# Kernel optimization log

Hardware: AMD Instinct MI355X
Metric: run time of the kernel (lower is better)

## Reference

```python
import jax, jax.numpy as jnp
import numpy as np

H = 128
NUM_IN = 384
B, N, K = 4, 2048, 48
SCALE = 30.0
EPS = 1e-5


def _layernorm(x, gamma, beta):
    mu = jnp.mean(x, axis=-1, keepdims=True)
    var = jnp.mean(jnp.square(x - mu), axis=-1, keepdims=True)
    return (x - mu) * jax.lax.rsqrt(var + EPS) * gamma + beta


def setup_inputs() -> dict:
    key = jax.random.key(0)
    ks = jax.random.split(key, 12)
    s = lambda fan_in: 1.0 / np.sqrt(fan_in)
    inp = {
        "h_V": jax.random.normal(ks[0], (B, N, H), jnp.float32),
        "h_E": jax.random.normal(ks[1], (B, N, K, NUM_IN), jnp.float32),
        "mask_V": jnp.ones((B, N), jnp.float32),
        "mask_attend": jnp.ones((B, N, K), jnp.float32),
        # message MLP
        "W1": jax.random.uniform(ks[2], (H + NUM_IN, H), jnp.float32, -s(H + NUM_IN), s(H + NUM_IN)),
        "b1": jnp.zeros((H,), jnp.float32),
        "W2": jax.random.uniform(ks[3], (H, H), jnp.float32, -s(H), s(H)),
        "b2": jnp.zeros((H,), jnp.float32),
        "W3": jax.random.uniform(ks[4], (H, H), jnp.float32, -s(H), s(H)),
        "b3": jnp.zeros((H,), jnp.float32),
        # layernorms
        "g1": jnp.ones((H,), jnp.float32), "be1": jnp.zeros((H,), jnp.float32),
        "g2": jnp.ones((H,), jnp.float32), "be2": jnp.zeros((H,), jnp.float32),
        # FFN
        "Wi": jax.random.uniform(ks[5], (H, 4 * H), jnp.float32, -s(H), s(H)),
        "bi": jnp.zeros((4 * H,), jnp.float32),
        "Wo": jax.random.uniform(ks[6], (4 * H, H), jnp.float32, -s(4 * H), s(4 * H)),
        "bo": jnp.zeros((H,), jnp.float32),
        # rezero alpha (init 0.01)
        "alpha": jnp.array([0.01], jnp.float32),
    }
    return inp


def reference(h_V, h_E, mask_V, mask_attend, W1, b1, W2, b2, W3, b3,
              g1, be1, g2, be2, Wi, bi, Wo, bo, alpha):
    gelu = lambda x: jax.nn.gelu(x, approximate=False)
    # broadcast-concat node features onto each neighbor edge: [B,N,K,H+num_in]
    h_V_expand = jnp.broadcast_to(h_V[:, :, None, :], (*h_E.shape[:-1], h_V.shape[-1]))
    h_EV = jnp.concatenate([h_V_expand, h_E], axis=-1)
    # 3-layer message MLP
    h_message = gelu(jnp.einsum("bnkf,fh->bnkh", h_EV, W1) + b1)
    h_message = gelu(jnp.einsum("bnkh,hg->bnkg", h_message, W2) + b2)
    h_message = jnp.einsum("bnkg,gh->bnkh", h_message, W3) + b3
    h_message = mask_attend[..., None] * h_message
    # masked sum-reduce over neighbors
    dh = jnp.sum(h_message, axis=-2) / SCALE
    # residual (rezero) + LayerNorm  (dropout = identity in eval)
    h = _layernorm(alpha * dh + h_V, g1, be1)
    # position-wise FFN
    dh = gelu(h @ Wi + bi) @ Wo + bo
    h = _layernorm(alpha * dh + h, g2, be2)
    # node mask
    h = mask_V[..., None] * h
    return h
```

## Files before the change

### kernel.cpp

```cpp
#include <hip/hip_runtime.h>

#define LN_EPS 1e-5f
#define RSCALE (1.0f / 30.0f)

typedef short short8  __attribute__((ext_vector_type(8)));
typedef short short4v __attribute__((ext_vector_type(4)));
typedef float f32x4   __attribute__((ext_vector_type(4)));

__device__ __forceinline__ unsigned short f2bf(float f) {
    unsigned u = __builtin_bit_cast(unsigned, f);
    u = u + 0x7FFFu + ((u >> 16) & 1u);
    return (unsigned short)(u >> 16);
}

__device__ __forceinline__ float gelu_f(float x) {
    float u  = 0.7978845608028654f * (x + 0.044715f * x * x * x);
    float e  = __expf(-2.0f * fabsf(u));
    float t  = 1.0f - 2.0f * e / (1.0f + e);
    return 0.5f * x * (1.0f + copysignf(t, u));
}

__device__ __forceinline__ short8 cvt8(float4 a, float4 b) {
    short8 r;
    r[0] = (short)f2bf(a.x); r[1] = (short)f2bf(a.y);
    r[2] = (short)f2bf(a.z); r[3] = (short)f2bf(a.w);
    r[4] = (short)f2bf(b.x); r[5] = (short)f2bf(b.y);
    r[6] = (short)f2bf(b.z); r[7] = (short)f2bf(b.w);
    return r;
}

__device__ __forceinline__ f32x4 zero4() {
    f32x4 v; v.x = 0.f; v.y = 0.f; v.z = 0.f; v.w = 0.f; return v;
}

__global__ __launch_bounds__(256) void prep_w(
    const float* __restrict__ W1, const float* __restrict__ W2,
    const float* __restrict__ W3,
    unsigned short* __restrict__ w1t, unsigned short* __restrict__ w2t,
    unsigned short* __restrict__ w3t)
{
    int t = blockIdx.x * 256 + threadIdx.x;
    if (t < 65536) {
        int m = t & 127, k = t >> 7;
        w1t[m * 512 + k] = f2bf(W1[k * 128 + m]);
    } else if (t < 81920) {
        int u = t - 65536, m = u & 127, k = u >> 7;
        w2t[m * 128 + k] = f2bf(W2[k * 128 + m]);
    } else if (t < 98304) {
        int u = t - 81920, m = u & 127, k = u >> 7;
        w3t[m * 128 + k] = f2bf(W3[k * 128 + m]);
    }
}

__global__ __launch_bounds__(256, 2) void edge_mlp(
    const float* __restrict__ hV, const float* __restrict__ hE,
    const float* __restrict__ mAtt,
    const unsigned short* __restrict__ w1t, const unsigned short* __restrict__ w2t,
    const unsigned short* __restrict__ w3t,
    const float* __restrict__ b1, const float* __restrict__ b2,
    const float* __restrict__ b3, float* __restrict__ dh)
{
    __shared__ short Hs[4][48 * 128];

    const int tid  = threadIdx.x;
    const int wv   = tid >> 6;
    const int lane = tid & 63;
    const int ln   = lane & 15;
    const int kg   = lane >> 4;
    const int node = blockIdx.x * 4 + wv;
    short* Hw = &Hs[wv][0];

    f32x4 acc[8][3];

#pragma unroll
    for (int j = 0; j < 8; ++j) acc[j][0] = zero4();
#pragma unroll
    for (int ks = 0; ks < 4; ++ks) {
        const float* hp = hV + node * 128 + ks * 32 + kg * 8;
        float4 v0 = *(const float4*)hp;
        float4 v1 = *(const float4*)(hp + 4);
        short8 bf = cvt8(v0, v1);
#pragma unroll
        for (int j = 0; j < 8; ++j) {
            short8 af = *(const short8*)(w1t + (j * 16 + ln) * 512 + ks * 32 + kg * 8);
            acc[j][0] = __builtin_amdgcn_mfma_f32_16x16x32_bf16(af, bf, acc[j][0], 0, 0, 0);
        }
    }
#pragma unroll
    for (int j = 0; j < 8; ++j) { acc[j][1] = acc[j][0]; acc[j][2] = acc[j][0]; }

    float4 e0[3], e1[3];
#pragma unroll
    for (int i = 0; i < 3; ++i) {
        const float* p = hE + (node * 48 + 16 * i + ln) * 384 + kg * 8;
        e0[i] = *(const float4*)p;
        e1[i] = *(const float4*)(p + 4);
    }
    for (int ks = 4; ks < 16; ++ks) {
        float4 f0[3], f1[3];
        if (ks < 15) {
#pragma unroll
            for (int i = 0; i < 3; ++i) {
                const float* p = hE + (node * 48 + 16 * i + ln) * 384 + (ks - 3) * 32 + kg * 8;
                f0[i] = *(const float4*)p;
                f1[i] = *(const float4*)(p + 4);
            }
        }
        short8 bf[3];
#pragma unroll
        for (int i = 0; i < 3; ++i) bf[i] = cvt8(e0[i], e1[i]);
#pragma unroll
        for (int j = 0; j < 8; ++j) {
            short8 af = *(const short8*)(w1t + (j * 16 + ln) * 512 + ks * 32 + kg * 8);
#pragma unroll
            for (int i = 0; i < 3; ++i)
                acc[j][i] = __builtin_amdgcn_mfma_f32_16x16x32_bf16(af, bf[i], acc[j][i], 0, 0, 0);
        }
#pragma unroll
        for (int i = 0; i < 3; ++i) { e0[i] = f0[i]; e1[i] = f1[i]; }
    }

#pragma unroll
    for (int j = 0; j < 8; ++j) {
        const float4 bb = *(const float4*)(b1 + j * 16 + 4 * kg);
        const int blk0 = 2 * j + (kg >> 1);
        const int off  = 4 * (kg & 1);
#pragma unroll
        for (int i = 0; i < 3; ++i) {
            const int n = 16 * i + ln;
            short4v p;
            p.x = (short)f2bf(gelu_f(acc[j][i].x + bb.x));
            p.y = (short)f2bf(gelu_f(acc[j][i].y + bb.y));
            p.z = (short)f2bf(gelu_f(acc[j][i].z + bb.z));
            p.w = (short)f2bf(gelu_f(acc[j][i].w + bb.w));
            *(short4v*)&Hw[n * 128 + ((blk0 ^ (n & 7)) * 8) + off] = p;
        }
    }

    for (int L = 0; L < 2; ++L) {
        const unsigned short* wt = (L == 0) ? w2t : w3t;
        f32x4 a2[8][3];
#pragma unroll
        for (int j = 0; j < 8; ++j)
#pragma unroll
            for (int i = 0; i < 3; ++i) a2[j][i] = zero4();

#pragma unroll
        for (int c = 0; c < 4; ++c) {
            short8 hb[3];
#pragma unroll
            for (int i = 0; i < 3; ++i) {
                const int n = 16 * i + ln;
                const int blk = (c * 4 + kg) ^ (n & 7);
                hb[i] = *(const short8*)&Hw[n * 128 + blk * 8];
            }
#pragma unroll
            for (int j = 0; j < 8; ++j) {
                short8 af = *(const short8*)(wt + (j * 16 + ln) * 128 + c * 32 + kg * 8);
#pragma unroll
                for (int i = 0; i < 3; ++i)
                    a2[j][i] = __builtin_amdgcn_mfma_f32_16x16x32_bf16(af, hb[i], a2[j][i], 0, 0, 0);
            }
        }

        if (L == 0) {
#pragma unroll
            for (int j = 0; j < 8; ++j) {
                const float4 bb = *(const float4*)(b2 + j * 16 + 4 * kg);
                const int blk0 = 2 * j + (kg >> 1);
                const int off  = 4 * (kg & 1);
#pragma unroll
                for (int i = 0; i < 3; ++i) {
                    const int n = 16 * i + ln;
                    short4v p;
                    p.x = (short)f2bf(gelu_f(a2[j][i].x + bb.x));
                    p.y = (short)f2bf(gelu_f(a2[j][i].y + bb.y));
                    p.z = (short)f2bf(gelu_f(a2[j][i].z + bb.z));
                    p.w = (short)f2bf(gelu_f(a2[j][i].w + bb.w));
                    *(short4v*)&Hw[n * 128 + ((blk0 ^ (n & 7)) * 8) + off] = p;
                }
            }
        } else {
            float mk[3];
#pragma unroll
            for (int i = 0; i < 3; ++i) mk[i] = mAtt[node * 48 + 16 * i + ln];
#pragma unroll
            for (int j = 0; j < 8; ++j) {
                const float4 bb = *(const float4*)(b3 + j * 16 + 4 * kg);
                float s0 = 0.f, s1 = 0.f, s2 = 0.f, s3 = 0.f;
#pragma unroll
                for (int i = 0; i < 3; ++i) {
                    s0 += (a2[j][i].x + bb.x) * mk[i];
                    s1 += (a2[j][i].y + bb.y) * mk[i];
                    s2 += (a2[j][i].z + bb.z) * mk[i];
                    s3 += (a2[j][i].w + bb.w) * mk[i];
                }
#pragma unroll
                for (int off = 1; off < 16; off <<= 1) {
                    s0 += __shfl_xor(s0, off, 64);
                    s1 += __shfl_xor(s1, off, 64);
                    s2 += __shfl_xor(s2, off, 64);
                    s3 += __shfl_xor(s3, off, 64);
                }
                if (ln == 0) {
                    float4 o;
                    o.x = s0 * RSCALE; o.y = s1 * RSCALE;
                    o.z = s2 * RSCALE; o.w = s3 * RSCALE;
                    *(float4*)&dh[node * 128 + j * 16 + 4 * kg] = o;
                }
            }
        }
    }
}

__global__ __launch_bounds__(256, 2) void node_ffn(
    const float* __restrict__ hV, const float* __restrict__ dh,
    const float* __restrict__ maskV,
    const float* __restrict__ g1, const float* __restrict__ be1,
    const float* __restrict__ g2, const float* __restrict__ be2,
    const float* __restrict__ Wi, const float* __restrict__ bi,
    const float* __restrict__ Wo, const float* __restrict__ bo,
    const float* __restrict__ alphap, float* __restrict__ out)
{
    __shared__ float hbuf[16 * 132];
    __shared__ float hidb[16 * 516];
    __shared__ float obuf[16 * 132];

    const int tid = threadIdx.x;
    const float al = alphap[0];
    const int nb = blockIdx.x * 16;

    {
        const int m = tid >> 4, s = tid & 15;
        const int i0 = s * 8;
        const int base = (nb + m) * 128 + i0;
        float x[8];
        {
            float4 a0 = *(const float4*)(dh + base);
            float4 a1 = *(const float4*)(dh + base + 4);
            float4 v0 = *(const float4*)(hV + base);
            float4 v1 = *(const float4*)(hV + base + 4);
            x[0] = v0.x + al * a0.x; x[1] = v0.y + al * a0.y;
            x[2] = v0.z + al * a0.z; x[3] = v0.w + al * a0.w;
            x[4] = v1.x + al * a1.x; x[5] = v1.y + al * a1.y;
            x[6] = v1.z + al * a1.z; x[7] = v1.w + al * a1.w;
        }
        float sm = 0.f;
#pragma unroll
        for (int q = 0; q < 8; ++q) sm += x[q];
#pragma unroll
        for (int off = 1; off < 16; off <<= 1) sm += __shfl_xor(sm, off, 64);
        const float mu = sm * (1.0f / 128.0f);
        float vs = 0.f;
#pragma unroll
        for (int q = 0; q < 8; ++q) { float d = x[q] - mu; vs += d * d; }
#pragma unroll
        for (int off = 1; off < 16; off <<= 1) vs += __shfl_xor(vs, off, 64);
        const float rs = rsqrtf(vs * (1.0f / 128.0f) + LN_EPS);
#pragma unroll
        for (int q = 0; q < 8; ++q)
            hbuf[m * 132 + i0 + q] = (x[q] - mu) * rs * g1[i0 + q] + be1[i0 + q];
    }
    __syncthreads();

    {
        const int jg = tid & 127, mhh = tid >> 7;
        const int j4 = jg * 4;
        float acc[8][4];
#pragma unroll
        for (int mm = 0; mm < 8; ++mm)
#pragma unroll
            for (int jj = 0; jj < 4; ++jj) acc[mm][jj] = 0.f;
        for (int i0 = 0; i0 < 128; i0 += 4) {
            float4 w0 = *(const float4*)(Wi + (i0 + 0) * 512 + j4);
            float4 w1 = *(const float4*)(Wi + (i0 + 1) * 512 + j4);
            float4 w2 = *(const float4*)(Wi + (i0 + 2) * 512 + j4);
            float4 w3 = *(const float4*)(Wi + (i0 + 3) * 512 + j4);
#pragma unroll
            for (int mm = 0; mm < 8; ++mm) {
                float4 h4 = *(const float4*)&hbuf[(mhh * 8 + mm) * 132 + i0];
                acc[mm][0] += h4.x * w0.x + h4.y * w1.x + h4.z * w2.x + h4.w * w3.x;
                acc[mm][1] += h4.x * w0.y + h4.y * w1.y + h4.z * w2.y + h4.w * w3.y;
                acc[mm][2] += h4.x * w0.z + h4.y * w1.z + h4.z * w2.z + h4.w * w3.z;
                acc[mm][3] += h4.x * w0.w + h4.y * w1.w + h4.z * w2.w + h4.w * w3.w;
            }
        }
        float4 bb = *(const float4*)(bi + j4);
#pragma unroll
        for (int mm = 0; mm < 8; ++mm) {
            float4 o;
            o.x = gelu_f(acc[mm][0] + bb.x);
            o.y = gelu_f(acc[mm][1] + bb.y);
            o.z = gelu_f(acc[mm][2] + bb.z);
            o.w = gelu_f(acc[mm][3] + bb.w);
            *(float4*)&hidb[(mhh * 8 + mm) * 516 + j4] = o;
        }
    }
    __syncthreads();

    {
        const int m = tid >> 4;
        const int n8 = (tid & 15) * 8;
        float4 r0, r1;
        r0.x = r0.y = r0.z = r0.w = 0.f;
        r1.x = r1.y = r1.z = r1.w = 0.f;
        for (int j0 = 0; j0 < 512; j0 += 4) {
            float4 hh = *(const float4*)&hidb[m * 516 + j0];
            float hq[4] = {hh.x, hh.y, hh.z, hh.w};
#pragma unroll
            for (int jj = 0; jj < 4; ++jj) {
                float4 w0 = *(const float4*)(Wo + (j0 + jj) * 128 + n8);
                float4 w1 = *(const float4*)(Wo + (j0 + jj) * 128 + n8 + 4);
                r0.x += hq[jj] * w0.x; r0.y += hq[jj] * w0.y;
                r0.z += hq[jj] * w0.z; r0.w += hq[jj] * w0.w;
                r1.x += hq[jj] * w1.x; r1.y += hq[jj] * w1.y;
                r1.z += hq[jj] * w1.z; r1.w += hq[jj] * w1.w;
            }
        }
        float4 q0 = *(const float4*)(bo + n8);
        float4 q1 = *(const float4*)(bo + n8 + 4);
        r0.x += q0.x; r0.y += q0.y; r0.z += q0.z; r0.w += q0.w;
        r1.x += q1.x; r1.y += q1.y; r1.z += q1.z; r1.w += q1.w;
        *(float4*)&obuf[m * 132 + n8]     = r0;
        *(float4*)&obuf[m * 132 + n8 + 4] = r1;
    }
    __syncthreads();

    {
        const int m = tid >> 4, s = tid & 15;
        const int i0 = s * 8;
        float x[8];
#pragma unroll
        for (int q = 0; q < 8; ++q)
            x[q] = hbuf[m * 132 + i0 + q] + al * obuf[m * 132 + i0 + q];
        float sm = 0.f;
#pragma unroll
        for (int q = 0; q < 8; ++q) sm += x[q];
#pragma unroll
        for (int off = 1; off < 16; off <<= 1) sm += __shfl_xor(sm, off, 64);
        const float mu = sm * (1.0f / 128.0f);
        float vs = 0.f;
#pragma unroll
        for (int q = 0; q < 8; ++q) { float d = x[q] - mu; vs += d * d; }
#pragma unroll
        for (int off = 1; off < 16; off <<= 1) vs += __shfl_xor(vs, off, 64);
        const float rs = rsqrtf(vs * (1.0f / 128.0f) + LN_EPS);
        const float mk = maskV[nb + m];
        float y[8];
#pragma unroll
        for (int q = 0; q < 8; ++q)
            y[q] = ((x[q] - mu) * rs * g2[i0 + q] + be2[i0 + q]) * mk;
        float4 o0, o1;
        o0.x = y[0]; o0.y = y[1]; o0.z = y[2]; o0.w = y[3];
        o1.x = y[4]; o1.y = y[5]; o1.z = y[6]; o1.w = y[7];
        const int base = (nb + m) * 128 + i0;
        *(float4*)(out + base)     = o0;
        *(float4*)(out + base + 4) = o1;
    }
}

extern "C" void kernel_launch(void* const* d_in, const int* in_sizes, int n_in,
                              void* d_out, int out_size, void* d_ws, size_t ws_size,
                              hipStream_t stream)
{
    const float* hV  = (const float*)d_in[0];
    const float* hE  = (const float*)d_in[1];
    const float* mV  = (const float*)d_in[2];
    const float* mA  = (const float*)d_in[3];
    const float* W1  = (const float*)d_in[4];
    const float* b1  = (const float*)d_in[5];
    const float* W2  = (const float*)d_in[6];
    const float* b2  = (const float*)d_in[7];
    const float* W3  = (const float*)d_in[8];
    const float* b3  = (const float*)d_in[9];
    const float* g1  = (const float*)d_in[10];
    const float* be1 = (const float*)d_in[11];
    const float* g2  = (const float*)d_in[12];
    const float* be2 = (const float*)d_in[13];
    const float* Wi  = (const float*)d_in[14];
    const float* bi  = (const float*)d_in[15];
    const float* Wo  = (const float*)d_in[16];
    const float* bo  = (const float*)d_in[17];
    const float* al  = (const float*)d_in[18];
    float* out = (float*)d_out;

    float* dh = (float*)d_ws;
    unsigned short* w1t = (unsigned short*)((char*)d_ws + (size_t)4194304);
    unsigned short* w2t = w1t + 65536;
    unsigned short* w3t = w2t + 16384;

    prep_w  <<<384,  256, 0, stream>>>(W1, W2, W3, w1t, w2t, w3t);
    edge_mlp<<<2048, 256, 0, stream>>>(hV, hE, mA, w1t, w2t, w3t, b1, b2, b3, dh);
    node_ffn<<<512,  256, 0, stream>>>(hV, dh, mV, g1, be1, g2, be2, Wi, bi, Wo, bo, al, out);
}
```

Measured before the change: 1.066 ms.

## Stage edge features via global_load_lds and split output columns across wave pairs

```diff
diff --git a/kernel.cpp b/kernel.cpp
--- a/kernel.cpp
+++ b/kernel.cpp
@@ -31,6 +31,12 @@
 
 __device__ __forceinline__ f32x4 zero4() {
     f32x4 v; v.x = 0.f; v.y = 0.f; v.z = 0.f; v.w = 0.f; return v;
+}
+
+__device__ __forceinline__ void gl_lds16(const float* g, float* l) {
+    __builtin_amdgcn_global_load_lds(
+        (const __attribute__((address_space(1))) void*)g,
+        (__attribute__((address_space(3))) void*)l, 16, 0, 0);
 }
 
 __global__ __launch_bounds__(256) void prep_w(
@@ -52,7 +58,7 @@
     }
 }
 
-__global__ __launch_bounds__(256, 2) void edge_mlp(
+__global__ __launch_bounds__(256, 3) void edge_mlp(
     const float* __restrict__ hV, const float* __restrict__ hE,
     const float* __restrict__ mAtt,
     const unsigned short* __restrict__ w1t, const unsigned short* __restrict__ w2t,
@@ -60,70 +66,87 @@
     const float* __restrict__ b1, const float* __restrict__ b2,
     const float* __restrict__ b3, float* __restrict__ dh)
 {
-    __shared__ short Hs[4][48 * 128];
+    __shared__ __align__(16) float Abuf[96 * 32];
+    __shared__ __align__(16) short Hs[2][48 * 128];
+    __shared__ float mb[96];
 
     const int tid  = threadIdx.x;
     const int wv   = tid >> 6;
     const int lane = tid & 63;
     const int ln   = lane & 15;
     const int kg   = lane >> 4;
-    const int node = blockIdx.x * 4 + wv;
-    short* Hw = &Hs[wv][0];
-
-    f32x4 acc[8][3];
-
-#pragma unroll
-    for (int j = 0; j < 8; ++j) acc[j][0] = zero4();
-#pragma unroll
-    for (int ks = 0; ks < 4; ++ks) {
-        const float* hp = hV + node * 128 + ks * 32 + kg * 8;
-        float4 v0 = *(const float4*)hp;
-        float4 v1 = *(const float4*)(hp + 4);
-        short8 bf = cvt8(v0, v1);
-#pragma unroll
-        for (int j = 0; j < 8; ++j) {
-            short8 af = *(const short8*)(w1t + (j * 16 + ln) * 512 + ks * 32 + kg * 8);
-            acc[j][0] = __builtin_amdgcn_mfma_f32_16x16x32_bf16(af, bf, acc[j][0], 0, 0, 0);
-        }
-    }
-#pragma unroll
-    for (int j = 0; j < 8; ++j) { acc[j][1] = acc[j][0]; acc[j][2] = acc[j][0]; }
-
-    float4 e0[3], e1[3];
-#pragma unroll
-    for (int i = 0; i < 3; ++i) {
-        const float* p = hE + (node * 48 + 16 * i + ln) * 384 + kg * 8;
-        e0[i] = *(const float4*)p;
-        e1[i] = *(const float4*)(p + 4);
-    }
-    for (int ks = 4; ks < 16; ++ks) {
-        float4 f0[3], f1[3];
-        if (ks < 15) {
-#pragma unroll
-            for (int i = 0; i < 3; ++i) {
-                const float* p = hE + (node * 48 + 16 * i + ln) * 384 + (ks - 3) * 32 + kg * 8;
-                f0[i] = *(const float4*)p;
-                f1[i] = *(const float4*)(p + 4);
-            }
-        }
+    const int nl   = wv >> 1;
+    const int mh   = wv & 1;
+    const int node = blockIdx.x * 2 + nl;
+    const int base_row = blockIdx.x * 96;
+    short* Hw = &Hs[nl][0];
+
+    if (tid < 96) mb[tid] = mAtt[base_row + tid];
+
+    f32x4 acc[4][3];
+
+#pragma unroll
+    for (int j = 0; j < 4; ++j) acc[j][0] = zero4();
+    {
+        float4 hv[8];
+#pragma unroll
+        for (int ks = 0; ks < 4; ++ks) {
+            const float* p = hV + node * 128 + ks * 32 + kg * 8;
+            hv[2 * ks]     = *(const float4*)p;
+            hv[2 * ks + 1] = *(const float4*)(p + 4);
+        }
+#pragma unroll
+        for (int ks = 0; ks < 4; ++ks) {
+            short8 bfv = cvt8(hv[2 * ks], hv[2 * ks + 1]);
+#pragma unroll
+            for (int j = 0; j < 4; ++j) {
+                const int m = (mh * 4 + j) * 16 + ln;
+                short8 af = *(const short8*)(w1t + (size_t)m * 512 + ks * 32 + kg * 8);
+                acc[j][0] = __builtin_amdgcn_mfma_f32_16x16x32_bf16(af, bfv, acc[j][0], 0, 0, 0);
+            }
+        }
+    }
+#pragma unroll
+    for (int j = 0; j < 4; ++j) { acc[j][1] = acc[j][0]; acc[j][2] = acc[j][0]; }
+
+    for (int c = 0; c < 12; ++c) {
+        if (c) __syncthreads();
+#pragma unroll
+        for (int q = 0; q < 3; ++q) {
+            const int o   = q * 256 + tid;
+            const int row = o >> 3, u = o & 7;
+            const int ku  = u ^ (row & 7);
+            const float* g = hE + (size_t)(base_row + row) * 384 + c * 32 + ku * 4;
+            gl_lds16(g, &Abuf[o * 4]);
+        }
+        __syncthreads();
+
         short8 bf[3];
 #pragma unroll
-        for (int i = 0; i < 3; ++i) bf[i] = cvt8(e0[i], e1[i]);
-#pragma unroll
-        for (int j = 0; j < 8; ++j) {
-            short8 af = *(const short8*)(w1t + (j * 16 + ln) * 512 + ks * 32 + kg * 8);
+        for (int i = 0; i < 3; ++i) {
+            const int row = nl * 48 + 16 * i + ln;
+            const int u0 = (2 * kg)     ^ (row & 7);
+            const int u1 = (2 * kg + 1) ^ (row & 7);
+            float4 x0 = *(const float4*)&Abuf[row * 32 + u0 * 4];
+            float4 x1 = *(const float4*)&Abuf[row * 32 + u1 * 4];
+            bf[i] = cvt8(x0, x1);
+        }
+#pragma unroll
+        for (int j = 0; j < 4; ++j) {
+            const int m = (mh * 4 + j) * 16 + ln;
+            short8 af = *(const short8*)(w1t + (size_t)m * 512 + 128 + c * 32 + kg * 8);
 #pragma unroll
             for (int i = 0; i < 3; ++i)
                 acc[j][i] = __builtin_amdgcn_mfma_f32_16x16x32_bf16(af, bf[i], acc[j][i], 0, 0, 0);
         }
-#pragma unroll
-        for (int i = 0; i < 3; ++i) { e0[i] = f0[i]; e1[i] = f1[i]; }
-    }
-
-#pragma unroll
-    for (int j = 0; j < 8; ++j) {
-        const float4 bb = *(const float4*)(b1 + j * 16 + 4 * kg);
-        const int blk0 = 2 * j + (kg >> 1);
+    }
+    __syncthreads();
+
+#pragma unroll
+    for (int j = 0; j < 4; ++j) {
+        const int J  = mh * 4 + j;
+        const float4 bb = *(const float4*)(b1 + J * 16 + 4 * kg);
+        const int blk0 = 2 * J + (kg >> 1);
         const int off  = 4 * (kg & 1);
 #pragma unroll
         for (int i = 0; i < 3; ++i) {
@@ -136,38 +159,42 @@
             *(short4v*)&Hw[n * 128 + ((blk0 ^ (n & 7)) * 8) + off] = p;
         }
     }
+    __syncthreads();
 
     for (int L = 0; L < 2; ++L) {
         const unsigned short* wt = (L == 0) ? w2t : w3t;
-        f32x4 a2[8][3];
-#pragma unroll
-        for (int j = 0; j < 8; ++j)
+        f32x4 a2[4][3];
+#pragma unroll
+        for (int j = 0; j < 4; ++j)
 #pragma unroll
             for (int i = 0; i < 3; ++i) a2[j][i] = zero4();
 
 #pragma unroll
-        for (int c = 0; c < 4; ++c) {
+        for (int c2 = 0; c2 < 4; ++c2) {
             short8 hb[3];
 #pragma unroll
             for (int i = 0; i < 3; ++i) {
                 const int n = 16 * i + ln;
-                const int blk = (c * 4 + kg) ^ (n & 7);
+                const int blk = (c2 * 4 + kg) ^ (n & 7);
                 hb[i] = *(const short8*)&Hw[n * 128 + blk * 8];
             }
 #pragma unroll
-            for (int j = 0; j < 8; ++j) {
-                short8 af = *(const short8*)(wt + (j * 16 + ln) * 128 + c * 32 + kg * 8);
+            for (int j = 0; j < 4; ++j) {
+                const int m = (mh * 4 + j) * 16 + ln;
+                short8 af = *(const short8*)(wt + (size_t)m * 128 + c2 * 32 + kg * 8);
 #pragma unroll
                 for (int i = 0; i < 3; ++i)
                     a2[j][i] = __builtin_amdgcn_mfma_f32_16x16x32_bf16(af, hb[i], a2[j][i], 0, 0, 0);
             }
         }
+        __syncthreads();
 
         if (L == 0) {
 #pragma unroll
-            for (int j = 0; j < 8; ++j) {
-                const float4 bb = *(const float4*)(b2 + j * 16 + 4 * kg);
-                const int blk0 = 2 * j + (kg >> 1);
+            for (int j = 0; j < 4; ++j) {
+                const int J  = mh * 4 + j;
+                const float4 bb = *(const float4*)(b2 + J * 16 + 4 * kg);
+                const int blk0 = 2 * J + (kg >> 1);
                 const int off  = 4 * (kg & 1);
 #pragma unroll
                 for (int i = 0; i < 3; ++i) {
@@ -180,13 +207,15 @@
                     *(short4v*)&Hw[n * 128 + ((blk0 ^ (n & 7)) * 8) + off] = p;
                 }
             }
+            __syncthreads();
         } else {
             float mk[3];
 #pragma unroll
-            for (int i = 0; i < 3; ++i) mk[i] = mAtt[node * 48 + 16 * i + ln];
-#pragma unroll
-            for (int j = 0; j < 8; ++j) {
-                const float4 bb = *(const float4*)(b3 + j * 16 + 4 * kg);
+            for (int i = 0; i < 3; ++i) mk[i] = mb[nl * 48 + 16 * i + ln];
+#pragma unroll
+            for (int j = 0; j < 4; ++j) {
+                const int J = mh * 4 + j;
+                const float4 bb = *(const float4*)(b3 + J * 16 + 4 * kg);
                 float s0 = 0.f, s1 = 0.f, s2 = 0.f, s3 = 0.f;
 #pragma unroll
                 for (int i = 0; i < 3; ++i) {
@@ -206,7 +235,7 @@
                     float4 o;
                     o.x = s0 * RSCALE; o.y = s1 * RSCALE;
                     o.z = s2 * RSCALE; o.w = s3 * RSCALE;
-                    *(float4*)&dh[node * 128 + j * 16 + 4 * kg] = o;
+                    *(float4*)&dh[node * 128 + J * 16 + 4 * kg] = o;
                 }
             }
         }
@@ -390,6 +419,6 @@
     unsigned short* w3t = w2t + 16384;
 
     prep_w  <<<384,  256, 0, stream>>>(W1, W2, W3, w1t, w2t, w3t);
-    edge_mlp<<<2048, 256, 0, stream>>>(hV, hE, mA, w1t, w2t, w3t, b1, b2, b3, dh);
+    edge_mlp<<<4096, 256, 0, stream>>>(hV, hE, mA, w1t, w2t, w3t, b1, b2, b3, dh);
     node_ffn<<<512,  256, 0, stream>>>(hV, dh, mV, g1, be1, g2, be2, Wi, bi, Wo, bo, al, out);
 }
```

After: 1.028 ms. 3.6% less time.
